# Optimization experiments

Hardware: AMD Instinct MI355X
Metric: run time of the kernel (lower is better)

The kernel has to match this reference:

```python
import jax, jax.numpy as jnp
import numpy as np

DROPOUT_P = 0.1


def setup_inputs() -> dict:
    key = jax.random.key(0)
    kq, kk, kv = jax.random.split(key, 3)
    B, S, E = 16, 2048, 128
    return {
        "query": jax.random.normal(kq, (B, S, E), dtype=jnp.float32),
        "key": jax.random.normal(kk, (B, S, E), dtype=jnp.float32),
        "value": jax.random.normal(kv, (B, S, E), dtype=jnp.float32),
    }


def reference(query, key, value):
    # attn_weights = softmax(Q K^T)  -- note: NO 1/sqrt(d) scaling in the original module
    scores = jnp.einsum("bqe,bke->bqk", query, key)  # [B, S, S]
    attn = jax.nn.softmax(scores, axis=-1)
    # dropout (training mode, p=DROPOUT_P), deterministic fixed key
    dkey = jax.random.key(42)
    keep = jax.random.bernoulli(dkey, 1.0 - DROPOUT_P, attn.shape)
    attn = jnp.where(keep, attn / (1.0 - DROPOUT_P), 0.0).astype(attn.dtype)
    return jnp.einsum("bqk,bke->bqe", attn, value)
```

## Files before the change

### kernel.cpp

```cpp
#include <hip/hip_runtime.h>
#include <hip/hip_bf16.h>
#include <stdint.h>

#define S_LEN 2048
#define E_DIM 128
#define KT 32
#define KTM 64

#define ARR_BYTES    (8u * 1024 * 1024)
#define PART2_FLOATS 16640
#define TIER_B       ((size_t)3u * ARR_BYTES)
#define TIER_A2      (TIER_B + (size_t)512 * PART2_FLOATS * 4)
#define TIER_A4      (TIER_B + (size_t)1024 * PART2_FLOATS * 4)

typedef __attribute__((ext_vector_type(4))) float f32x4;
typedef __attribute__((ext_vector_type(4))) short s16x4;
typedef __attribute__((ext_vector_type(8))) short bf16x8;

__device__ __forceinline__ short f2bf(float f) {
    uint32_t u = __builtin_bit_cast(uint32_t, f);
    u += 0x7FFFu + ((u >> 16) & 1u);
    return (short)(u >> 16);
}
__device__ __forceinline__ float bf2f(short h) {
    uint32_t u = ((uint32_t)(uint16_t)h) << 16;
    return __builtin_bit_cast(float, u);
}
__device__ __forceinline__ uint32_t cvtpk_bf16(float lo, float hi) {
    uint32_t d;
    asm volatile("v_cvt_pk_bf16_f32 %0, %1, %2" : "=v"(d) : "v"(lo), "v"(hi));
    return d;
}

__device__ __forceinline__ void threefry_g(uint32_t k0, uint32_t k1,
                                           uint32_t c0, uint32_t c1,
                                           uint32_t& y0, uint32_t& y1) {
    uint32_t ks2 = k0 ^ k1 ^ 0x1BD11BDAu;
    uint32_t x0 = c0 + k0, x1 = c1 + k1;
#define TF_R(rr) { x0 += x1; x1 = __builtin_amdgcn_alignbit(x1, x1, 32u - rr); x1 ^= x0; }
    TF_R(13) TF_R(15) TF_R(26) TF_R(6)
    x0 += k1;  x1 += ks2 + 1u;
    TF_R(17) TF_R(29) TF_R(16) TF_R(24)
    x0 += ks2; x1 += k0 + 2u;
    TF_R(13) TF_R(15) TF_R(26) TF_R(6)
    x0 += k0;  x1 += k1 + 3u;
    TF_R(17) TF_R(29) TF_R(16) TF_R(24)
    x0 += k1;  x1 += ks2 + 4u;
    TF_R(13) TF_R(15) TF_R(26) TF_R(6)
    x0 += ks2; x1 += k0 + 5u;
#undef TF_R
    y0 = x0; y1 = x1;
}

__device__ __forceinline__ bool keep_bit(uint32_t j) {
    uint32_t y0, y1;
    threefry_g(0u, 42u, 0u, j, y0, y1);
    return (y0 ^ y1) < 0xE6666600u;
}

__global__ __launch_bounds__(256, 4)
void convert_kv(const float* __restrict__ Kg, const float* __restrict__ Vg,
                short* __restrict__ KH, short* __restrict__ KL,
                short* __restrict__ VT) {
    __shared__ short vs[64][130];
    const int blk = blockIdx.x;
    const int b = blk >> 5, t = blk & 31;
    const size_t base = ((size_t)b * S_LEN + (size_t)t * 64) * E_DIM;
    const int e0 = (threadIdx.x & 31) * 4;
    const int rb = threadIdx.x >> 5;
    #pragma unroll
    for (int it = 0; it < 8; ++it) {
        int row = it * 8 + rb;
        f32x4 kv = *(const f32x4*)(Kg + base + row * E_DIM + e0);
        s16x4 h, lo;
        #pragma unroll
        for (int i = 0; i < 4; ++i) {
            short hh = f2bf(kv[i]);
            h[i]  = hh;
            lo[i] = f2bf(kv[i] - bf2f(hh));
        }
        *(s16x4*)(KH + base + row * E_DIM + e0) = h;
        *(s16x4*)(KL + base + row * E_DIM + e0) = lo;
        f32x4 vv = *(const f32x4*)(Vg + base + row * E_DIM + e0);
        #pragma unroll
        for (int i = 0; i < 4; ++i) vs[row][e0 + i] = f2bf(vv[i]);
    }
    __syncthreads();
    const int e = threadIdx.x >> 1;
    const int k2 = (threadIdx.x & 1) * 32;
    short* dst = VT + ((size_t)b * E_DIM + e) * S_LEN + t * 64 + k2;
    #pragma unroll
    for (int i = 0; i < 32; i += 4) {
        s16x4 v;
        #pragma unroll
        for (int q2 = 0; q2 < 4; ++q2) v[q2] = vs[k2 + i + q2][e];
        *(s16x4*)(dst + i) = v;
    }
}

template<int NSPLIT>
__global__ __launch_bounds__(512, 4)
void attn9(const float* __restrict__ Qg, const short* __restrict__ KH,
           const short* __restrict__ KL, const short* __restrict__ VT,
           float* __restrict__ outp) {
    constexpr int NT = (S_LEN / NSPLIT) / KT;
    __shared__ __attribute__((aligned(16))) short kh[KT * E_DIM];
    __shared__ __attribute__((aligned(16))) short kl[KT * E_DIM];
    __shared__ __attribute__((aligned(16))) short vt[E_DIM * 40];
    __shared__ __attribute__((aligned(16))) uint32_t plt[8][16 * 20];
    __shared__ uint32_t mldsT[NT][128];

    const int tid = threadIdx.x;
    const int w   = tid >> 6;
    const int ln  = tid & 63;
    const int r   = ln & 15;
    const int g   = ln >> 4;
    const int nwg = 256 * NSPLIT;
    const int wg  = (blockIdx.x & 7) * (nwg >> 3) + (blockIdx.x >> 3);
    const int t   = wg / NSPLIT;
    const int s   = wg % NSPLIT;
    const int b   = t >> 4;
    const int q0  = (t & 15) << 7;
    const int k0g = s * (S_LEN / NSPLIT);
    const size_t boff = (size_t)b * S_LEN * E_DIM;

    bf16x8 qh[4], ql[4];
    #pragma unroll
    for (int ec = 0; ec < 4; ++ec) {
        const float* src = Qg + boff + (size_t)(q0 + w * 16 + r) * E_DIM + ec * 32 + g * 8;
        f32x4 va = *(const f32x4*)(src);
        f32x4 vb2 = *(const f32x4*)(src + 4);
        #pragma unroll
        for (int i = 0; i < 4; ++i) {
            short hh = f2bf(va[i]);
            qh[ec][i] = hh;
            ql[ec][i] = f2bf(va[i] - bf2f(hh));
            short h2 = f2bf(vb2[i]);
            qh[ec][4 + i] = h2;
            ql[ec][4 + i] = f2bf(vb2[i] - bf2f(h2));
        }
    }

    {
        const int segs = (S_LEN / NSPLIT) / 64;
        const uint32_t jb = (((uint32_t)b << 11) + (uint32_t)q0) * 2048u
                          + (uint32_t)k0g + (uint32_t)ln;
        for (int i = 0; i < 16 * segs; ++i) {
            int rr  = w * 16 + i / segs;
            int seg = i % segs;
            uint32_t j = jb + (uint32_t)rr * 2048u + (uint32_t)(seg * 64);
            uint64_t m = __ballot(keep_bit(j));
            if (ln < 2) mldsT[seg * 2 + ln][rr] = (uint32_t)(m >> (ln * 32));
        }
    }

    const short* KHb = KH + ((size_t)b * S_LEN + k0g) * E_DIM;
    const short* KLb = KL + ((size_t)b * S_LEN + k0g) * E_DIM;
    const short* VTb = VT + (size_t)b * E_DIM * S_LEN + k0g;

    bf16x8 skh, skl, svv;
    const int se0 = (tid & 15) * 8;
    const int srl = tid >> 4;
    const int sve = tid >> 2;
    const int svq = tid & 3;
#define LOAD_TILE(ktt)                                                          \
    {                                                                           \
        skh = *(const bf16x8*)(KHb + (size_t)((ktt) * KT + srl) * E_DIM + se0); \
        skl = *(const bf16x8*)(KLb + (size_t)((ktt) * KT + srl) * E_DIM + se0); \
        svv = *(const bf16x8*)(VTb + (size_t)sve * S_LEN + (ktt) * KT + svq * 8); \
    }
    LOAD_TILE(0)

    f32x4 oacc[8];
    #pragma unroll
    for (int i = 0; i < 8; ++i) oacc[i] = f32x4{0.f, 0.f, 0.f, 0.f};
    float mrun = -1e30f, den = 0.f;

    for (int kt = 0; kt < NT; ++kt) {
        __syncthreads();
        {
            int idx = (srl * E_DIM + se0) ^ ((srl & 7) << 3);
            *(bf16x8*)(kh + idx) = skh;
            *(bf16x8*)(kl + idx) = skl;
            const int swv = ((sve >> 3) & 1) << 1;
            *(bf16x8*)(vt + sve * 40 + ((svq ^ swv) << 3)) = svv;
        }
        __syncthreads();

        f32x4 sc[2];
        #pragma unroll
        for (int c = 0; c < 2; ++c) {
            f32x4 acc = f32x4{0.f, 0.f, 0.f, 0.f};
            int krow = c * 16 + r;
            int sw = (krow & 7) << 3;
            #pragma unroll
            for (int ec = 0; ec < 4; ++ec) {
                int idx = (krow * E_DIM + ec * 32 + g * 8) ^ sw;
                bf16x8 bh = *(const bf16x8*)(kh + idx);
                bf16x8 bl = *(const bf16x8*)(kl + idx);
                acc = __builtin_amdgcn_mfma_f32_16x16x32_bf16(bh, qh[ec], acc, 0, 0, 0);
                acc = __builtin_amdgcn_mfma_f32_16x16x32_bf16(bl, qh[ec], acc, 0, 0, 0);
                acc = __builtin_amdgcn_mfma_f32_16x16x32_bf16(bh, ql[ec], acc, 0, 0, 0);
            }
            sc[c] = acc;
        }

        float pmax = fmaxf(fmaxf(fmaxf(sc[0][0], sc[0][1]), fmaxf(sc[0][2], sc[0][3])),
                           fmaxf(fmaxf(sc[1][0], sc[1][1]), fmaxf(sc[1][2], sc[1][3])));
        pmax = fmaxf(pmax, __shfl_xor(pmax, 16));
        pmax = fmaxf(pmax, __shfl_xor(pmax, 32));
        if (__any(pmax - mrun > 8.0f)) {
            float mnew = fmaxf(mrun, pmax);
            float scl = __expf(mrun - mnew);
            mrun = mnew;
            den *= scl;
            #pragma unroll
            for (int et = 0; et < 8; ++et) oacc[et] *= scl;
        }
        float rs = 0.f;
        #pragma unroll
        for (int c = 0; c < 2; ++c) {
            #pragma unroll
            for (int reg = 0; reg < 4; ++reg) {
                float p = __expf(sc[c][reg] - mrun);
                sc[c][reg] = p;
                rs += p;
            }
        }
        rs += __shfl_xor(rs, 16);
        rs += __shfl_xor(rs, 32);
        den += rs;

        if (kt + 1 < NT) LOAD_TILE(kt + 1)

        uint32_t bits = mldsT[kt][w * 16 + r] >> (g * 4);
        float pm[2][4];
        #pragma unroll
        for (int c = 0; c < 2; ++c) {
            #pragma unroll
            for (int reg = 0; reg < 4; ++reg)
                pm[c][reg] = ((bits >> (c * 16 + reg)) & 1u)
                               ? sc[c][reg] * (1.0f / 0.9f) : 0.0f;
        }
        uint2 pk0 = { cvtpk_bf16(pm[0][0], pm[0][1]), cvtpk_bf16(pm[0][2], pm[0][3]) };
        uint2 pk1 = { cvtpk_bf16(pm[1][0], pm[1][1]), cvtpk_bf16(pm[1][2], pm[1][3]) };
        *(uint2*)(&plt[w][r * 20 + g * 2])     = pk0;
        *(uint2*)(&plt[w][r * 20 + 8 + g * 2]) = pk1;
        bf16x8 pfrag = *(const bf16x8*)((const short*)&plt[w][0] + r * 40 + g * 8);

        const int swr = ((r >> 3) & 1) << 1;
        #pragma unroll
        for (int et = 0; et < 8; ++et) {
            const short* vp = vt + (et * 16 + r) * 40 + ((g ^ swr) << 3);
            bf16x8 av = *(const bf16x8*)vp;
            oacc[et] = __builtin_amdgcn_mfma_f32_16x16x32_bf16(av, pfrag, oacc[et], 0, 0, 0);
        }
    }

    const int q = w * 16 + r;
    if (NSPLIT == 1) {
        float inv = 1.0f / den;
        float* dst = outp + boff + (size_t)(q0 + q) * E_DIM;
        #pragma unroll
        for (int et = 0; et < 8; ++et) {
            f32x4 o = oacc[et] * inv;
            *(f32x4*)(dst + et * 16 + g * 4) = o;
        }
    } else {
        float* pb = outp + (size_t)wg * PART2_FLOATS;
        if (g == 0) {
            pb[q]       = mrun;
            pb[128 + q] = den;
        }
        #pragma unroll
        for (int et = 0; et < 8; ++et)
            *(f32x4*)(pb + 256 + q * E_DIM + et * 16 + g * 4) = oacc[et];
    }
}

template<int NSPLIT>
__global__ __launch_bounds__(256, 8)
void merge9(const float* __restrict__ part, float* __restrict__ Og) {
    const int t = blockIdx.x;
    const int b = t >> 4;
    const int q0 = (t & 15) << 7;
    const float* ps[NSPLIT];
    #pragma unroll
    for (int s = 0; s < NSPLIT; ++s)
        ps[s] = part + (size_t)(t * NSPLIT + s) * PART2_FLOATS;
    float* dst = Og + (size_t)b * S_LEN * E_DIM + (size_t)q0 * E_DIM;
    for (int i = 0; i < 64; ++i) {
        int idx = i * 256 + threadIdx.x;
        int row = idx >> 7, e = idx & 127;
        float mm = ps[0][row];
        #pragma unroll
        for (int s = 1; s < NSPLIT; ++s) mm = fmaxf(mm, ps[s][row]);
        float d = 0.f, o = 0.f;
        #pragma unroll
        for (int s = 0; s < NSPLIT; ++s) {
            float sc = __expf(ps[s][row] - mm);
            d += ps[s][128 + row] * sc;
            o += ps[s][256 + row * E_DIM + e] * sc;
        }
        dst[row * E_DIM + e] = o / d;
    }
}

__global__ __launch_bounds__(256, 2)
void attn_mono(const float* __restrict__ Qg, const float* __restrict__ Kg,
               const float* __restrict__ Vg, float* __restrict__ Og) {
    __shared__ short kh[KTM * E_DIM];
    __shared__ short kl[KTM * E_DIM];
    __shared__ short vt[E_DIM * 66];
    __shared__ short pl[4][16 * 64];

    const int tid = threadIdx.x;
    const int w   = tid >> 6;
    const int ln  = tid & 63;
    const int r   = ln & 15;
    const int g   = ln >> 4;
    const int bid = blockIdx.x;
    const int b   = bid >> 5;
    const int q0  = (bid & 31) << 6;
    const size_t boff = (size_t)b * S_LEN * E_DIM;

    {
        const float* src = Qg + boff + (size_t)q0 * E_DIM;
        const int e0 = (tid & 31) * 4;
        const int rb = tid >> 5;
        #pragma unroll
        for (int it = 0; it < 8; ++it) {
            int row = it * 8 + rb;
            f32x4 v = *(const f32x4*)(src + row * E_DIM + e0);
            s16x4 h, lo;
            #pragma unroll
            for (int i = 0; i < 4; ++i) {
                short hh = f2bf(v[i]);
                h[i]  = hh;
                lo[i] = f2bf(v[i] - bf2f(hh));
            }
            int idx = (row * E_DIM + e0) ^ ((row & 7) << 3);
            *(s16x4*)(kh + idx) = h;
            *(s16x4*)(kl + idx) = lo;
        }
    }
    __syncthreads();
    bf16x8 qh[4], ql[4];
    {
        int row = w * 16 + r;
        #pragma unroll
        for (int ec = 0; ec < 4; ++ec) {
            int idx = (row * E_DIM + ec * 32 + g * 8) ^ ((row & 7) << 3);
            qh[ec] = *(const bf16x8*)(kh + idx);
            ql[ec] = *(const bf16x8*)(kl + idx);
        }
    }
    f32x4 oacc[8];
    #pragma unroll
    for (int i = 0; i < 8; ++i) oacc[i] = f32x4{0.f, 0.f, 0.f, 0.f};
    float mrun[4] = {-1e30f, -1e30f, -1e30f, -1e30f};
    float den[4]  = {0.f, 0.f, 0.f, 0.f};

    for (int kt = 0; kt < S_LEN / KTM; ++kt) {
        __syncthreads();
        {
            const float* src = Kg + boff + (size_t)(kt * KTM) * E_DIM;
            const int e0 = (tid & 31) * 4;
            const int rb = tid >> 5;
            #pragma unroll
            for (int it = 0; it < 8; ++it) {
                int row = it * 8 + rb;
                f32x4 v = *(const f32x4*)(src + row * E_DIM + e0);
                s16x4 h, lo;
                #pragma unroll
                for (int i = 0; i < 4; ++i) {
                    short hh = f2bf(v[i]);
                    h[i]  = hh;
                    lo[i] = f2bf(v[i] - bf2f(hh));
                }
                int idx = (row * E_DIM + e0) ^ ((row & 7) << 3);
                *(s16x4*)(kh + idx) = h;
                *(s16x4*)(kl + idx) = lo;
            }
        }
        {
            const float* src = Vg + boff + (size_t)(kt * KTM) * E_DIM;
            const int e0 = (tid & 31) * 4;
            const int kb = (tid >> 5) * 2;
            #pragma unroll
            for (int it = 0; it < 4; ++it) {
                int k = it * 16 + kb;
                f32x4 a  = *(const f32x4*)(src + k * E_DIM + e0);
                f32x4 c2 = *(const f32x4*)(src + (k + 1) * E_DIM + e0);
                #pragma unroll
                for (int ci = 0; ci < 4; ++ci) {
                    uint32_t pack = (uint32_t)(uint16_t)f2bf(a[ci]) |
                                    ((uint32_t)(uint16_t)f2bf(c2[ci]) << 16);
                    *(uint32_t*)(vt + (e0 + ci) * 66 + k) = pack;
                }
            }
        }
        __syncthreads();
        f32x4 sc[4];
        #pragma unroll
        for (int c = 0; c < 4; ++c) {
            f32x4 acc = f32x4{0.f, 0.f, 0.f, 0.f};
            int krow = c * 16 + r;
            int sw = (krow & 7) << 3;
            #pragma unroll
            for (int ec = 0; ec < 4; ++ec) {
                int idx = (krow * E_DIM + ec * 32 + g * 8) ^ sw;
                bf16x8 bh = *(const bf16x8*)(kh + idx);
                bf16x8 bl = *(const bf16x8*)(kl + idx);
                acc = __builtin_amdgcn_mfma_f32_16x16x32_bf16(qh[ec], bh, acc, 0, 0, 0);
                acc = __builtin_amdgcn_mfma_f32_16x16x32_bf16(ql[ec], bh, acc, 0, 0, 0);
                acc = __builtin_amdgcn_mfma_f32_16x16x32_bf16(qh[ec], bl, acc, 0, 0, 0);
            }
            sc[c] = acc;
        }
        float scale[4];
        #pragma unroll
        for (int reg = 0; reg < 4; ++reg) {
            float v0 = fmaxf(fmaxf(sc[0][reg], sc[1][reg]),
                             fmaxf(sc[2][reg], sc[3][reg]));
            v0 = fmaxf(v0, __shfl_xor(v0, 1));
            v0 = fmaxf(v0, __shfl_xor(v0, 2));
            v0 = fmaxf(v0, __shfl_xor(v0, 4));
            v0 = fmaxf(v0, __shfl_xor(v0, 8));
            float mnew = fmaxf(mrun[reg], v0);
            scale[reg] = __expf(mrun[reg] - mnew);
            mrun[reg] = mnew;
        }
        float rs[4] = {0.f, 0.f, 0.f, 0.f};
        #pragma unroll
        for (int c = 0; c < 4; ++c) {
            #pragma unroll
            for (int reg = 0; reg < 4; ++reg) {
                float p = __expf(sc[c][reg] - mrun[reg]);
                sc[c][reg] = p;
                rs[reg] += p;
            }
        }
        #pragma unroll
        for (int reg = 0; reg < 4; ++reg) {
            float v0 = rs[reg];
            v0 += __shfl_xor(v0, 1);
            v0 += __shfl_xor(v0, 2);
            v0 += __shfl_xor(v0, 4);
            v0 += __shfl_xor(v0, 8);
            den[reg] = den[reg] * scale[reg] + v0;
        }
        #pragma unroll
        for (int et = 0; et < 8; ++et) {
            #pragma unroll
            for (int reg = 0; reg < 4; ++reg) oacc[et][reg] *= scale[reg];
        }
        #pragma unroll
        for (int c = 0; c < 4; ++c) {
            int kcol = kt * KTM + c * 16 + r;
            #pragma unroll
            for (int reg = 0; reg < 4; ++reg) {
                int row = g * 4 + reg;
                uint32_t q = (uint32_t)(q0 + w * 16 + row);
                uint32_t j = (((uint32_t)b << 11) + q) * 2048u + (uint32_t)kcol;
                float pm = keep_bit(j) ? sc[c][reg] * (1.0f / 0.9f) : 0.0f;
                int idx = (row * 64 + (c * 16 + r)) ^ ((row & 7) << 3);
                pl[w][idx] = f2bf(pm);
            }
        }
        bf16x8 pa[2];
        #pragma unroll
        for (int st = 0; st < 2; ++st) {
            int idx = (r * 64 + st * 32 + g * 8) ^ ((r & 7) << 3);
            pa[st] = *(const bf16x8*)(&pl[w][0] + idx);
        }
        #pragma unroll
        for (int et = 0; et < 8; ++et) {
            int e = et * 16 + r;
            f32x4 o = oacc[et];
            #pragma unroll
            for (int st = 0; st < 2; ++st) {
                union { bf16x8 v; uint32_t u[4]; } vb;
                #pragma unroll
                for (int i2 = 0; i2 < 4; ++i2)
                    vb.u[i2] = *(const uint32_t*)(vt + e * 66 + st * 32 + g * 8 + i2 * 2);
                o = __builtin_amdgcn_mfma_f32_16x16x32_bf16(pa[st], vb.v, o, 0, 0, 0);
            }
            oacc[et] = o;
        }
    }
    float inv[4];
    #pragma unroll
    for (int reg = 0; reg < 4; ++reg) inv[reg] = 1.0f / den[reg];
    float* dst = Og + boff + (size_t)q0 * E_DIM;
    #pragma unroll
    for (int et = 0; et < 8; ++et) {
        #pragma unroll
        for (int reg = 0; reg < 4; ++reg) {
            int row = w * 16 + g * 4 + reg;
            int e = et * 16 + r;
            dst[row * E_DIM + e] = oacc[et][reg] * inv[reg];
        }
    }
}

extern "C" void kernel_launch(void* const* d_in, const int* in_sizes, int n_in,
                              void* d_out, int out_size, void* d_ws, size_t ws_size,
                              hipStream_t stream) {
    (void)in_sizes; (void)n_in; (void)out_size;
    const float* Q = (const float*)d_in[0];
    const float* K = (const float*)d_in[1];
    const float* V = (const float*)d_in[2];
    float* O = (float*)d_out;
    if (ws_size >= TIER_B) {
        short* KH = (short*)d_ws;
        short* KL = (short*)((char*)d_ws + ARR_BYTES);
        short* VT = (short*)((char*)d_ws + 2u * ARR_BYTES);
        hipLaunchKernelGGL(convert_kv, dim3(512), dim3(256), 0, stream, K, V, KH, KL, VT);
        if (ws_size >= TIER_A4) {
            float* part = (float*)((char*)d_ws + TIER_B);
            hipLaunchKernelGGL((attn9<4>), dim3(1024), dim3(512), 0, stream,
                               Q, KH, KL, VT, part);
            hipLaunchKernelGGL((merge9<4>), dim3(256), dim3(256), 0, stream, part, O);
        } else if (ws_size >= TIER_A2) {
            float* part = (float*)((char*)d_ws + TIER_B);
            hipLaunchKernelGGL((attn9<2>), dim3(512), dim3(512), 0, stream,
                               Q, KH, KL, VT, part);
            hipLaunchKernelGGL((merge9<2>), dim3(256), dim3(256), 0, stream, part, O);
        } else {
            hipLaunchKernelGGL((attn9<1>), dim3(256), dim3(512), 0, stream,
                               Q, KH, KL, VT, O);
        }
    } else {
        hipLaunchKernelGGL(attn_mono, dim3(512), dim3(256), 0, stream, Q, K, V, O);
    }
}
```

Measured before the change: 221.7 us.

## Replace LDS P-fragment transpose with cross-lane shuffles and defer dropout scale

The P fragment is now built from the MFMA score layout with cross-lane shuffles, removing the per-warp LDS staging buffer. The 1/0.9 dropout scale moves from every probability to the final normalisation. The mask-generation loop is restructured with a compile-time segment count, and launch bounds ask for 8 waves per SIMD. The goal is to cut LDS traffic and per-element multiplies and to allow higher occupancy, at the cost of eight extra shuffles per tile and more register pressure under the tighter launch bound.

```diff
diff --git a/kernel.cpp b/kernel.cpp
--- a/kernel.cpp
+++ b/kernel.cpp
@@ -99,15 +99,14 @@
 }
 
 template<int NSPLIT>
-__global__ __launch_bounds__(512, 4)
-void attn9(const float* __restrict__ Qg, const short* __restrict__ KH,
-           const short* __restrict__ KL, const short* __restrict__ VT,
-           float* __restrict__ outp) {
+__global__ __launch_bounds__(512, 8)
+void attn10(const float* __restrict__ Qg, const short* __restrict__ KH,
+            const short* __restrict__ KL, const short* __restrict__ VT,
+            float* __restrict__ outp) {
     constexpr int NT = (S_LEN / NSPLIT) / KT;
     __shared__ __attribute__((aligned(16))) short kh[KT * E_DIM];
     __shared__ __attribute__((aligned(16))) short kl[KT * E_DIM];
     __shared__ __attribute__((aligned(16))) short vt[E_DIM * 40];
-    __shared__ __attribute__((aligned(16))) uint32_t plt[8][16 * 20];
     __shared__ uint32_t mldsT[NT][128];
 
     const int tid = threadIdx.x;
@@ -142,15 +141,16 @@
     }
 
     {
-        const int segs = (S_LEN / NSPLIT) / 64;
+        constexpr int segs = (S_LEN / NSPLIT) / 64;
         const uint32_t jb = (((uint32_t)b << 11) + (uint32_t)q0) * 2048u
                           + (uint32_t)k0g + (uint32_t)ln;
-        for (int i = 0; i < 16 * segs; ++i) {
-            int rr  = w * 16 + i / segs;
-            int seg = i % segs;
-            uint32_t j = jb + (uint32_t)rr * 2048u + (uint32_t)(seg * 64);
-            uint64_t m = __ballot(keep_bit(j));
-            if (ln < 2) mldsT[seg * 2 + ln][rr] = (uint32_t)(m >> (ln * 32));
+        for (int rr = 0; rr < 16; ++rr) {
+            uint32_t jrow = jb + (uint32_t)(w * 16 + rr) * 2048u;
+            #pragma unroll
+            for (int seg = 0; seg < segs; ++seg) {
+                uint64_t m = __ballot(keep_bit(jrow + (uint32_t)(seg * 64)));
+                if (ln < 2) mldsT[seg * 2 + ln][w * 16 + rr] = (uint32_t)(m >> (ln * 32));
+            }
         }
     }
 
@@ -234,19 +234,35 @@
         if (kt + 1 < NT) LOAD_TILE(kt + 1)
 
         uint32_t bits = mldsT[kt][w * 16 + r] >> (g * 4);
-        float pm[2][4];
+        float pmv[2][4];
         #pragma unroll
         for (int c = 0; c < 2; ++c) {
             #pragma unroll
             for (int reg = 0; reg < 4; ++reg)
-                pm[c][reg] = ((bits >> (c * 16 + reg)) & 1u)
-                               ? sc[c][reg] * (1.0f / 0.9f) : 0.0f;
-        }
-        uint2 pk0 = { cvtpk_bf16(pm[0][0], pm[0][1]), cvtpk_bf16(pm[0][2], pm[0][3]) };
-        uint2 pk1 = { cvtpk_bf16(pm[1][0], pm[1][1]), cvtpk_bf16(pm[1][2], pm[1][3]) };
-        *(uint2*)(&plt[w][r * 20 + g * 2])     = pk0;
-        *(uint2*)(&plt[w][r * 20 + 8 + g * 2]) = pk1;
-        bf16x8 pfrag = *(const bf16x8*)((const short*)&plt[w][0] + r * 40 + g * 8);
+                pmv[c][reg] = ((bits >> (c * 16 + reg)) & 1u) ? sc[c][reg] : 0.0f;
+        }
+        uint32_t W0 = cvtpk_bf16(pmv[0][0], pmv[0][1]);
+        uint32_t W1 = cvtpk_bf16(pmv[0][2], pmv[0][3]);
+        uint32_t W2 = cvtpk_bf16(pmv[1][0], pmv[1][1]);
+        uint32_t W3 = cvtpk_bf16(pmv[1][2], pmv[1][3]);
+
+        const int s01 = ((g & 1) << 5) + r;
+        const int s23 = s01 + 16;
+        uint32_t a0 = (uint32_t)__shfl((int)W0, s01);
+        uint32_t a2 = (uint32_t)__shfl((int)W2, s01);
+        uint32_t b0 = (uint32_t)__shfl((int)W1, s01);
+        uint32_t b2 = (uint32_t)__shfl((int)W3, s01);
+        uint32_t c0 = (uint32_t)__shfl((int)W0, s23);
+        uint32_t c2 = (uint32_t)__shfl((int)W2, s23);
+        uint32_t d0 = (uint32_t)__shfl((int)W1, s23);
+        uint32_t d2 = (uint32_t)__shfl((int)W3, s23);
+        union { bf16x8 v; uint32_t u[4]; } pf;
+        const bool lo = (g < 2);
+        pf.u[0] = lo ? a0 : a2;
+        pf.u[1] = lo ? b0 : b2;
+        pf.u[2] = lo ? c0 : c2;
+        pf.u[3] = lo ? d0 : d2;
+        bf16x8 pfrag = pf.v;
 
         const int swr = ((r >> 3) & 1) << 1;
         #pragma unroll
@@ -259,7 +275,7 @@
 
     const int q = w * 16 + r;
     if (NSPLIT == 1) {
-        float inv = 1.0f / den;
+        float inv = (1.0f / 0.9f) / den;
         float* dst = outp + boff + (size_t)(q0 + q) * E_DIM;
         #pragma unroll
         for (int et = 0; et < 8; ++et) {
@@ -302,7 +318,7 @@
             d += ps[s][128 + row] * sc;
             o += ps[s][256 + row * E_DIM + e] * sc;
         }
-        dst[row * E_DIM + e] = o / d;
+        dst[row * E_DIM + e] = (o / d) * (1.0f / 0.9f);
     }
 }
 
@@ -519,16 +535,16 @@
         hipLaunchKernelGGL(convert_kv, dim3(512), dim3(256), 0, stream, K, V, KH, KL, VT);
         if (ws_size >= TIER_A4) {
             float* part = (float*)((char*)d_ws + TIER_B);
-            hipLaunchKernelGGL((attn9<4>), dim3(1024), dim3(512), 0, stream,
+            hipLaunchKernelGGL((attn10<4>), dim3(1024), dim3(512), 0, stream,
                                Q, KH, KL, VT, part);
             hipLaunchKernelGGL((merge9<4>), dim3(256), dim3(256), 0, stream, part, O);
         } else if (ws_size >= TIER_A2) {
             float* part = (float*)((char*)d_ws + TIER_B);
-            hipLaunchKernelGGL((attn9<2>), dim3(512), dim3(512), 0, stream,
+            hipLaunchKernelGGL((attn10<2>), dim3(512), dim3(512), 0, stream,
                                Q, KH, KL, VT, part);
             hipLaunchKernelGGL((merge9<2>), dim3(256), dim3(256), 0, stream, part, O);
         } else {
-            hipLaunchKernelGGL((attn9<1>), dim3(256), dim3(512), 0, stream,
+            hipLaunchKernelGGL((attn10<1>), dim3(256), dim3(512), 0, stream,
                                Q, KH, KL, VT, O);
         }
     } else {
```

Measured after the change: 797.3 us. +259.6%, slower.
